# Performance work log

Hardware: AMD Instinct MI355X
Metric: run time of the kernel (lower is better)

Reference implementation:

```python
import jax, jax.numpy as jnp
import numpy as np

B, H, L, D = 2, 16, 2048, 64
SCALE = 1.0 / np.sqrt(D).astype(np.float32)

def setup_inputs() -> dict:
    key = jax.random.key(0)
    kq, kk, kv = jax.random.split(key, 3)
    q = jax.random.normal(kq, (B, H, L, D), dtype=jnp.float32)
    k = jax.random.normal(kk, (B, H, L, D), dtype=jnp.float32)
    v = jax.random.normal(kv, (B, H, L, D), dtype=jnp.float32)
    return {"q": q, "k": k, "v": v}

def reference(q, k, v):
    # scores: [B, H, L_q, L_k]
    attention = jnp.einsum('bhqd,bhkd->bhqk', q, k) * SCALE
    attention = jax.nn.softmax(attention, axis=-1)
    # dropout p=0.0 -> identity
    context = jnp.einsum('bhqk,bhkd->bhqd', attention, v)
    return (context, attention)
```

## Files before the change

kernel.cpp:

```cpp
#include <hip/hip_runtime.h>
#include <stdint.h>


#define L_SEQ 2048
#define D_HEAD 64
#define N_BH   32
#define BQ     64
#define BK     64
#define NT     256

typedef float f32x4 __attribute__((ext_vector_type(4)));
typedef short s16x8 __attribute__((ext_vector_type(8)));

#define MFMA16(A, B, C) __builtin_amdgcn_mfma_f32_16x16x32_bf16((A), (B), (C), 0, 0, 0)

__device__ __forceinline__ unsigned int bf16_rne_u(float x) {
    union { float f; unsigned int u; } c; c.f = x;
    return (c.u + 0x7FFFu + ((c.u >> 16) & 1u)) >> 16;
}
__device__ __forceinline__ float bf16_f32(unsigned int h) {
    union { unsigned int u; float f; } c; c.u = h << 16;
    return c.f;
}

__global__ __launch_bounds__(NT, 2)
void sdpa_mfma_kernel(const float* __restrict__ qg,
                      const float* __restrict__ kg,
                      const float* __restrict__ vg,
                      float* __restrict__ ctx,
                      float* __restrict__ attn)
{
    extern __shared__ char lds[];
    char*  SH = lds;
    char*  SL = lds + 8192;
    float* PS = (float*)(lds + 16384);

    const int t    = threadIdx.x;
    const int lane = t & 63;
    const int wid  = t >> 6;
    const int c    = lane & 15;
    const int g    = lane >> 4;

    const int bh = blockIdx.y;
    const int q0 = blockIdx.x * BQ;

    const float* qb = qg + (size_t)bh * L_SEQ * D_HEAD;
    const float* kb = kg + (size_t)bh * L_SEQ * D_HEAD;
    const float* vb = vg + (size_t)bh * L_SEQ * D_HEAD;

    float* PSw = PS + wid * (16 * 68);

    s16x8 qhi[2], qlo[2];
    {
        const float* qr = qb + (size_t)(q0 + wid * 16 + c) * D_HEAD + g * 8;
        #pragma unroll
        for (int kf = 0; kf < 2; ++kf) {
            float4 a = *(const float4*)(qr + kf * 32);
            float4 b = *(const float4*)(qr + kf * 32 + 4);
            float v[8] = {a.x, a.y, a.z, a.w, b.x, b.y, b.z, b.w};
            #pragma unroll
            for (int i = 0; i < 8; ++i) {
                unsigned int h = bf16_rne_u(v[i]);
                qhi[kf][i] = (short)h;
                qlo[kf][i] = (short)bf16_rne_u(v[i] - bf16_f32(h));
            }
        }
    }

    float rs[4] = {0.f, 0.f, 0.f, 0.f};

    #pragma unroll 1
    for (int kt = 0; kt < L_SEQ / BK; ++kt) {
        __syncthreads();
        {
            const float* kt0 = kb + (size_t)kt * BK * D_HEAD;
            #pragma unroll
            for (int ii = 0; ii < 4; ++ii) {
                int idx = ii * NT + t;
                int r = idx >> 4, c4 = idx & 15;
                float4 val = ((const float4*)(kt0 + (size_t)r * D_HEAD))[c4];
                ushort4 h;
                h.x = (unsigned short)bf16_rne_u(val.x);
                h.y = (unsigned short)bf16_rne_u(val.y);
                h.z = (unsigned short)bf16_rne_u(val.z);
                h.w = (unsigned short)bf16_rne_u(val.w);
                *(ushort4*)(SH + r * 128 + ((c4 * 8) ^ ((r & 7) << 4))) = h;
            }
        }
        __syncthreads();
        #pragma unroll
        for (int cg = 0; cg < 4; ++cg) {
            int j = cg * 16 + c;
            int key = (j & 7) << 4;
            const char* rh = SH + j * 128;
            s16x8 b0 = *(const s16x8*)(rh + ((g * 16) ^ key));
            s16x8 b1 = *(const s16x8*)(rh + ((64 + g * 16) ^ key));
            f32x4 s = {0.f, 0.f, 0.f, 0.f};
            s = MFMA16(qhi[0], b0, s);
            s = MFMA16(qhi[1], b1, s);
            #pragma unroll
            for (int r = 0; r < 4; ++r) rs[r] += __expf(s[r] * 0.125f);
        }
    }

    float inv[4];
    #pragma unroll
    for (int r = 0; r < 4; ++r) {
        float s = rs[r];
        s += __shfl_xor(s, 1); s += __shfl_xor(s, 2);
        s += __shfl_xor(s, 4); s += __shfl_xor(s, 8);
        inv[r] = 1.0f / s;
    }

    float* ab = attn + (size_t)(bh * L_SEQ + q0 + wid * 16) * L_SEQ;
    f32x4 cacc[4];
    #pragma unroll
    for (int cg = 0; cg < 4; ++cg) cacc[cg] = (f32x4){0.f, 0.f, 0.f, 0.f};

    #pragma unroll 1
    for (int kt = 0; kt < L_SEQ / BK; ++kt) {
        __syncthreads();
        {
            const float* kt0 = kb + (size_t)kt * BK * D_HEAD;
            #pragma unroll
            for (int ii = 0; ii < 4; ++ii) {
                int idx = ii * NT + t;
                int r = idx >> 4, c4 = idx & 15;
                float4 val = ((const float4*)(kt0 + (size_t)r * D_HEAD))[c4];
                ushort4 h, l;
                unsigned int hx = bf16_rne_u(val.x), hy = bf16_rne_u(val.y);
                unsigned int hz = bf16_rne_u(val.z), hw = bf16_rne_u(val.w);
                h.x = (unsigned short)hx; h.y = (unsigned short)hy;
                h.z = (unsigned short)hz; h.w = (unsigned short)hw;
                l.x = (unsigned short)bf16_rne_u(val.x - bf16_f32(hx));
                l.y = (unsigned short)bf16_rne_u(val.y - bf16_f32(hy));
                l.z = (unsigned short)bf16_rne_u(val.z - bf16_f32(hz));
                l.w = (unsigned short)bf16_rne_u(val.w - bf16_f32(hw));
                int off = r * 128 + ((c4 * 8) ^ ((r & 7) << 4));
                *(ushort4*)(SH + off) = h;
                *(ushort4*)(SL + off) = l;
            }
        }
        __syncthreads();
        #pragma unroll
        for (int cg = 0; cg < 4; ++cg) {
            int j = cg * 16 + c;
            int key = (j & 7) << 4;
            const char* rh = SH + j * 128;
            const char* rl = SL + j * 128;
            s16x8 bh0 = *(const s16x8*)(rh + ((g * 16) ^ key));
            s16x8 bh1 = *(const s16x8*)(rh + ((64 + g * 16) ^ key));
            s16x8 bl0 = *(const s16x8*)(rl + ((g * 16) ^ key));
            s16x8 bl1 = *(const s16x8*)(rl + ((64 + g * 16) ^ key));
            f32x4 s = {0.f, 0.f, 0.f, 0.f};
            s = MFMA16(qhi[0], bh0, s);
            s = MFMA16(qhi[1], bh1, s);
            s = MFMA16(qlo[0], bh0, s);
            s = MFMA16(qlo[1], bh1, s);
            s = MFMA16(qhi[0], bl0, s);
            s = MFMA16(qhi[1], bl1, s);
            #pragma unroll
            for (int r = 0; r < 4; ++r) {
                float p = __expf(s[r] * 0.125f) * inv[r];
                PSw[(g * 4 + r) * 68 + cg * 16 + c] = p;
            }
        }
        __syncthreads();
        {
            const float* vt0 = vb + (size_t)kt * BK * D_HEAD;
            #pragma unroll
            for (int ii = 0; ii < 2; ++ii) {
                int item = ii * NT + t;
                int d4 = item & 15, j2 = item >> 4;
                const float* r0 = vt0 + (size_t)(2 * j2) * D_HEAD + d4 * 4;
                float4 a = *(const float4*)r0;
                float4 b = *(const float4*)(r0 + D_HEAD);
                float av[4] = {a.x, a.y, a.z, a.w};
                float bv[4] = {b.x, b.y, b.z, b.w};
                #pragma unroll
                for (int i = 0; i < 4; ++i) {
                    int d = d4 * 4 + i;
                    unsigned int h0 = bf16_rne_u(av[i]);
                    unsigned int h1 = bf16_rne_u(bv[i]);
                    unsigned int l0 = bf16_rne_u(av[i] - bf16_f32(h0));
                    unsigned int l1 = bf16_rne_u(bv[i] - bf16_f32(h1));
                    int off = d * 128 + ((4 * j2) ^ ((d & 7) << 4));
                    *(unsigned int*)(SH + off) = h0 | (h1 << 16);
                    *(unsigned int*)(SL + off) = l0 | (l1 << 16);
                }
            }
        }
        __syncthreads();
        #pragma unroll
        for (int it = 0; it < 4; ++it) {
            int r2 = it * 4 + g;
            float4 pv = *(const float4*)(PSw + r2 * 68 + c * 4);
            *(float4*)(ab + (size_t)r2 * L_SEQ + kt * BK + c * 4) = pv;
        }
        s16x8 ph[2], pl[2];
        {
            const float* pr = PSw + c * 68;
            #pragma unroll
            for (int kf = 0; kf < 2; ++kf) {
                float4 a = *(const float4*)(pr + kf * 32 + g * 8);
                float4 b = *(const float4*)(pr + kf * 32 + g * 8 + 4);
                float v[8] = {a.x, a.y, a.z, a.w, b.x, b.y, b.z, b.w};
                #pragma unroll
                for (int i = 0; i < 8; ++i) {
                    unsigned int h = bf16_rne_u(v[i]);
                    ph[kf][i] = (short)h;
                    pl[kf][i] = (short)bf16_rne_u(v[i] - bf16_f32(h));
                }
            }
        }
        #pragma unroll
        for (int cg = 0; cg < 4; ++cg) {
            int d = cg * 16 + c;
            int key = (d & 7) << 4;
            const char* rh = SH + d * 128;
            const char* rl = SL + d * 128;
            s16x8 vh0 = *(const s16x8*)(rh + ((g * 16) ^ key));
            s16x8 vh1 = *(const s16x8*)(rh + ((64 + g * 16) ^ key));
            s16x8 vl0 = *(const s16x8*)(rl + ((g * 16) ^ key));
            s16x8 vl1 = *(const s16x8*)(rl + ((64 + g * 16) ^ key));
            f32x4 cc = cacc[cg];
            cc = MFMA16(ph[0], vh0, cc);
            cc = MFMA16(ph[1], vh1, cc);
            cc = MFMA16(pl[0], vh0, cc);
            cc = MFMA16(pl[1], vh1, cc);
            cc = MFMA16(ph[0], vl0, cc);
            cc = MFMA16(ph[1], vl1, cc);
            cacc[cg] = cc;
        }
    }

    float* cb = ctx + (size_t)(bh * L_SEQ + q0 + wid * 16) * D_HEAD;
    #pragma unroll
    for (int cg = 0; cg < 4; ++cg) {
        #pragma unroll
        for (int r = 0; r < 4; ++r) {
            cb[(size_t)(g * 4 + r) * D_HEAD + cg * 16 + c] = cacc[cg][r];
        }
    }
}

extern "C" void kernel_launch(void* const* d_in, const int* in_sizes, int n_in,
                              void* d_out, int out_size, void* d_ws, size_t ws_size,
                              hipStream_t stream) {
    const float* q = (const float*)d_in[0];
    const float* k = (const float*)d_in[1];
    const float* v = (const float*)d_in[2];
    float* ctx  = (float*)d_out;
    float* attn = ctx + (size_t)N_BH * L_SEQ * D_HEAD;

    dim3 grid(L_SEQ / BQ, N_BH);
    size_t smem = 16384 + (size_t)4 * 16 * 68 * sizeof(float);
    hipLaunchKernelGGL(sdpa_mfma_kernel, grid, dim3(NT), smem, stream,
                       q, k, v, ctx, attn);
}
```

Before: 778.0 us.

## Precompute bf16 hi/lo splits in a prep kernel and prefetch tiles into registers

Adds a prep kernel that converts Q, K and V into bf16 hi/lo planes in workspace once, with V stored transposed. The main kernel then loads these pre-split tiles instead of redoing the conversion in every query block. It also prefetches the next K/V tile into registers while computing the current one, drops two barriers per iteration by giving K and V their own LDS buffers, remaps block indices for L2 locality, and raises the occupancy hint to 3. The cost is an extra launch, extra workspace traffic, and more LDS per block.

```diff
diff --git a/kernel.cpp b/kernel.cpp
--- a/kernel.cpp
+++ b/kernel.cpp
@@ -8,11 +8,13 @@
 #define BQ     64
 #define BK     64
 #define NT     256
+#define NKT    (L_SEQ / BK)
+#define PLANE  ((size_t)N_BH * L_SEQ * D_HEAD)
 
 typedef float f32x4 __attribute__((ext_vector_type(4)));
 typedef short s16x8 __attribute__((ext_vector_type(8)));
 
-#define MFMA16(A, B, C) __builtin_amdgcn_mfma_f32_16x16x32_bf16((A), (B), (C), 0, 0, 0)
+#define MFMA16(A,B,C) __builtin_amdgcn_mfma_f32_16x16x32_bf16((A),(B),(C),0,0,0)
 
 __device__ __forceinline__ unsigned int bf16_rne_u(float x) {
     union { float f; unsigned int u; } c; c.f = x;
@@ -23,76 +25,146 @@
     return c.f;
 }
 
-__global__ __launch_bounds__(NT, 2)
-void sdpa_mfma_kernel(const float* __restrict__ qg,
-                      const float* __restrict__ kg,
-                      const float* __restrict__ vg,
-                      float* __restrict__ ctx,
-                      float* __restrict__ attn)
+__global__ __launch_bounds__(NT)
+void prep_kernel(const float* __restrict__ qg, const float* __restrict__ kg,
+                 const float* __restrict__ vg, unsigned short* __restrict__ W)
+{
+    __shared__ float VT[64][68];
+    const int t = threadIdx.x;
+    const int tile = blockIdx.x, bh = blockIdx.y;
+    const size_t tb = ((size_t)bh * L_SEQ + (size_t)tile * 64) * D_HEAD;
+
+    unsigned short* QH = W;
+    unsigned short* QL = W + PLANE;
+    unsigned short* KH = W + 2 * PLANE;
+    unsigned short* KL = W + 3 * PLANE;
+    unsigned short* VTH = W + 4 * PLANE + (size_t)bh * D_HEAD * L_SEQ;
+    unsigned short* VTL = W + 5 * PLANE + (size_t)bh * D_HEAD * L_SEQ;
+
+    #pragma unroll
+    for (int ii = 0; ii < 4; ++ii) {
+        int idx = ii * NT + t;
+        int r = idx >> 4, c4 = idx & 15;
+        size_t o = tb + (size_t)r * D_HEAD + c4 * 4;
+        {
+            float4 val = *(const float4*)(qg + o);
+            ushort4 h, l;
+            unsigned hx = bf16_rne_u(val.x), hy = bf16_rne_u(val.y);
+            unsigned hz = bf16_rne_u(val.z), hw = bf16_rne_u(val.w);
+            h.x = (unsigned short)hx; h.y = (unsigned short)hy;
+            h.z = (unsigned short)hz; h.w = (unsigned short)hw;
+            l.x = (unsigned short)bf16_rne_u(val.x - bf16_f32(hx));
+            l.y = (unsigned short)bf16_rne_u(val.y - bf16_f32(hy));
+            l.z = (unsigned short)bf16_rne_u(val.z - bf16_f32(hz));
+            l.w = (unsigned short)bf16_rne_u(val.w - bf16_f32(hw));
+            *(ushort4*)(QH + o) = h;
+            *(ushort4*)(QL + o) = l;
+        }
+        {
+            float4 val = *(const float4*)(kg + o);
+            ushort4 h, l;
+            unsigned hx = bf16_rne_u(val.x), hy = bf16_rne_u(val.y);
+            unsigned hz = bf16_rne_u(val.z), hw = bf16_rne_u(val.w);
+            h.x = (unsigned short)hx; h.y = (unsigned short)hy;
+            h.z = (unsigned short)hz; h.w = (unsigned short)hw;
+            l.x = (unsigned short)bf16_rne_u(val.x - bf16_f32(hx));
+            l.y = (unsigned short)bf16_rne_u(val.y - bf16_f32(hy));
+            l.z = (unsigned short)bf16_rne_u(val.z - bf16_f32(hz));
+            l.w = (unsigned short)bf16_rne_u(val.w - bf16_f32(hw));
+            *(ushort4*)(KH + o) = h;
+            *(ushort4*)(KL + o) = l;
+        }
+        {
+            float4 val = *(const float4*)(vg + o);
+            *(float4*)(&VT[r][c4 * 4]) = val;
+        }
+    }
+    __syncthreads();
+    #pragma unroll
+    for (int ii = 0; ii < 2; ++ii) {
+        int item = ii * NT + t;
+        int d = item >> 3, jc = item & 7;
+        s16x8 hv, lv;
+        #pragma unroll
+        for (int j = 0; j < 8; ++j) {
+            float x = VT[jc * 8 + j][d];
+            unsigned h = bf16_rne_u(x);
+            hv[j] = (short)h;
+            lv[j] = (short)bf16_rne_u(x - bf16_f32(h));
+        }
+        size_t o = (size_t)d * L_SEQ + (size_t)tile * 64 + jc * 8;
+        *(s16x8*)(VTH + o) = hv;
+        *(s16x8*)(VTL + o) = lv;
+    }
+}
+
+__global__ __launch_bounds__(NT, 3)
+void sdpa_main(const unsigned short* __restrict__ W,
+               float* __restrict__ ctx, float* __restrict__ attn)
 {
     extern __shared__ char lds[];
-    char*  SH = lds;
-    char*  SL = lds + 8192;
-    float* PS = (float*)(lds + 16384);
-
-    const int t    = threadIdx.x;
-    const int lane = t & 63;
-    const int wid  = t >> 6;
-    const int c    = lane & 15;
-    const int g    = lane >> 4;
-
-    const int bh = blockIdx.y;
-    const int q0 = blockIdx.x * BQ;
-
-    const float* qb = qg + (size_t)bh * L_SEQ * D_HEAD;
-    const float* kb = kg + (size_t)bh * L_SEQ * D_HEAD;
-    const float* vb = vg + (size_t)bh * L_SEQ * D_HEAD;
+    char* KHs = lds;
+    char* KLs = lds + 8192;
+    char* VHs = lds + 16384;
+    char* VLs = lds + 24576;
+    float* PS = (float*)(lds + 32768);
+
+    const int t = threadIdx.x;
+    const int lane = t & 63, wid = t >> 6;
+    const int c = lane & 15, g = lane >> 4;
+
+    const int orig = blockIdx.x;
+    const int wg = (orig & 7) * 128 + (orig >> 3);
+    const int bh = wg >> 5, qb = wg & 31;
+    const int q0 = qb * BQ;
+
+    const unsigned short* QH = W;
+    const unsigned short* QL = W + PLANE;
+    const unsigned short* KHb = W + 2 * PLANE + (size_t)bh * L_SEQ * D_HEAD;
+    const unsigned short* KLb = W + 3 * PLANE + (size_t)bh * L_SEQ * D_HEAD;
+    const unsigned short* VHb = W + 4 * PLANE + (size_t)bh * D_HEAD * L_SEQ;
+    const unsigned short* VLb = W + 5 * PLANE + (size_t)bh * D_HEAD * L_SEQ;
 
     float* PSw = PS + wid * (16 * 68);
 
     s16x8 qhi[2], qlo[2];
     {
-        const float* qr = qb + (size_t)(q0 + wid * 16 + c) * D_HEAD + g * 8;
-        #pragma unroll
-        for (int kf = 0; kf < 2; ++kf) {
-            float4 a = *(const float4*)(qr + kf * 32);
-            float4 b = *(const float4*)(qr + kf * 32 + 4);
-            float v[8] = {a.x, a.y, a.z, a.w, b.x, b.y, b.z, b.w};
-            #pragma unroll
-            for (int i = 0; i < 8; ++i) {
-                unsigned int h = bf16_rne_u(v[i]);
-                qhi[kf][i] = (short)h;
-                qlo[kf][i] = (short)bf16_rne_u(v[i] - bf16_f32(h));
-            }
-        }
-    }
+        size_t qo = ((size_t)bh * L_SEQ + q0 + wid * 16 + c) * D_HEAD + g * 8;
+        qhi[0] = *(const s16x8*)(QH + qo);
+        qhi[1] = *(const s16x8*)(QH + qo + 32);
+        qlo[0] = *(const s16x8*)(QL + qo);
+        qlo[1] = *(const s16x8*)(QL + qo + 32);
+    }
+
+    const int i0 = t, i1 = NT + t;
+    const int r0 = i0 >> 3, c0 = i0 & 7;
+    const int r1 = i1 >> 3, c1 = i1 & 7;
+    const int ld0 = r0 * 128 + ((c0 * 16) ^ ((r0 & 7) << 4));
+    const int ld1 = r1 * 128 + ((c1 * 16) ^ ((r1 & 7) << 4));
+    const size_t ks0 = (size_t)r0 * D_HEAD + c0 * 8;
+    const size_t ks1 = (size_t)r1 * D_HEAD + c1 * 8;
+    const size_t vs0 = (size_t)r0 * L_SEQ + c0 * 8;
+    const size_t vs1 = (size_t)r1 * L_SEQ + c1 * 8;
 
     float rs[4] = {0.f, 0.f, 0.f, 0.f};
+    uint4 pk0 = *(const uint4*)(KHb + ks0);
+    uint4 pk1 = *(const uint4*)(KHb + ks1);
 
     #pragma unroll 1
-    for (int kt = 0; kt < L_SEQ / BK; ++kt) {
+    for (int kt = 0; kt < NKT; ++kt) {
         __syncthreads();
-        {
-            const float* kt0 = kb + (size_t)kt * BK * D_HEAD;
-            #pragma unroll
-            for (int ii = 0; ii < 4; ++ii) {
-                int idx = ii * NT + t;
-                int r = idx >> 4, c4 = idx & 15;
-                float4 val = ((const float4*)(kt0 + (size_t)r * D_HEAD))[c4];
-                ushort4 h;
-                h.x = (unsigned short)bf16_rne_u(val.x);
-                h.y = (unsigned short)bf16_rne_u(val.y);
-                h.z = (unsigned short)bf16_rne_u(val.z);
-                h.w = (unsigned short)bf16_rne_u(val.w);
-                *(ushort4*)(SH + r * 128 + ((c4 * 8) ^ ((r & 7) << 4))) = h;
-            }
-        }
+        *(uint4*)(KHs + ld0) = pk0;
+        *(uint4*)(KHs + ld1) = pk1;
         __syncthreads();
+        if (kt + 1 < NKT) {
+            const unsigned short* kn = KHb + (size_t)(kt + 1) * BK * D_HEAD;
+            pk0 = *(const uint4*)(kn + ks0);
+            pk1 = *(const uint4*)(kn + ks1);
+        }
         #pragma unroll
         for (int cg = 0; cg < 4; ++cg) {
-            int j = cg * 16 + c;
-            int key = (j & 7) << 4;
-            const char* rh = SH + j * 128;
+            int j = cg * 16 + c, key = (j & 7) << 4;
+            const char* rh = KHs + j * 128;
             s16x8 b0 = *(const s16x8*)(rh + ((g * 16) ^ key));
             s16x8 b1 = *(const s16x8*)(rh + ((64 + g * 16) ^ key));
             f32x4 s = {0.f, 0.f, 0.f, 0.f};
@@ -102,7 +174,6 @@
             for (int r = 0; r < 4; ++r) rs[r] += __expf(s[r] * 0.125f);
         }
     }
-
     float inv[4];
     #pragma unroll
     for (int r = 0; r < 4; ++r) {
@@ -112,42 +183,40 @@
         inv[r] = 1.0f / s;
     }
 
-    float* ab = attn + (size_t)(bh * L_SEQ + q0 + wid * 16) * L_SEQ;
+    float* ab = attn + ((size_t)bh * L_SEQ + q0 + wid * 16) * (size_t)L_SEQ;
     f32x4 cacc[4];
     #pragma unroll
     for (int cg = 0; cg < 4; ++cg) cacc[cg] = (f32x4){0.f, 0.f, 0.f, 0.f};
 
+    uint4 kh0 = *(const uint4*)(KHb + ks0), kh1 = *(const uint4*)(KHb + ks1);
+    uint4 kl0 = *(const uint4*)(KLb + ks0), kl1 = *(const uint4*)(KLb + ks1);
+    uint4 vh0 = *(const uint4*)(VHb + vs0), vh1 = *(const uint4*)(VHb + vs1);
+    uint4 vl0 = *(const uint4*)(VLb + vs0), vl1 = *(const uint4*)(VLb + vs1);
+
     #pragma unroll 1
-    for (int kt = 0; kt < L_SEQ / BK; ++kt) {
+    for (int kt = 0; kt < NKT; ++kt) {
         __syncthreads();
-        {
-            const float* kt0 = kb + (size_t)kt * BK * D_HEAD;
-            #pragma unroll
-            for (int ii = 0; ii < 4; ++ii) {
-                int idx = ii * NT + t;
-                int r = idx >> 4, c4 = idx & 15;
-                float4 val = ((const float4*)(kt0 + (size_t)r * D_HEAD))[c4];
-                ushort4 h, l;
-                unsigned int hx = bf16_rne_u(val.x), hy = bf16_rne_u(val.y);
-                unsigned int hz = bf16_rne_u(val.z), hw = bf16_rne_u(val.w);
-                h.x = (unsigned short)hx; h.y = (unsigned short)hy;
-                h.z = (unsigned short)hz; h.w = (unsigned short)hw;
-                l.x = (unsigned short)bf16_rne_u(val.x - bf16_f32(hx));
-                l.y = (unsigned short)bf16_rne_u(val.y - bf16_f32(hy));
-                l.z = (unsigned short)bf16_rne_u(val.z - bf16_f32(hz));
-                l.w = (unsigned short)bf16_rne_u(val.w - bf16_f32(hw));
-                int off = r * 128 + ((c4 * 8) ^ ((r & 7) << 4));
-                *(ushort4*)(SH + off) = h;
-                *(ushort4*)(SL + off) = l;
-            }
-        }
+        *(uint4*)(KHs + ld0) = kh0;  *(uint4*)(KHs + ld1) = kh1;
+        *(uint4*)(KLs + ld0) = kl0;  *(uint4*)(KLs + ld1) = kl1;
+        *(uint4*)(VHs + ld0) = vh0;  *(uint4*)(VHs + ld1) = vh1;
+        *(uint4*)(VLs + ld0) = vl0;  *(uint4*)(VLs + ld1) = vl1;
         __syncthreads();
+        if (kt + 1 < NKT) {
+            const unsigned short* knh = KHb + (size_t)(kt + 1) * BK * D_HEAD;
+            const unsigned short* knl = KLb + (size_t)(kt + 1) * BK * D_HEAD;
+            kh0 = *(const uint4*)(knh + ks0);  kh1 = *(const uint4*)(knh + ks1);
+            kl0 = *(const uint4*)(knl + ks0);  kl1 = *(const uint4*)(knl + ks1);
+            const unsigned short* vnh = VHb + (size_t)(kt + 1) * BK;
+            const unsigned short* vnl = VLb + (size_t)(kt + 1) * BK;
+            vh0 = *(const uint4*)(vnh + vs0);  vh1 = *(const uint4*)(vnh + vs1);
+            vl0 = *(const uint4*)(vnl + vs0);  vl1 = *(const uint4*)(vnl + vs1);
+        }
+
         #pragma unroll
         for (int cg = 0; cg < 4; ++cg) {
-            int j = cg * 16 + c;
-            int key = (j & 7) << 4;
-            const char* rh = SH + j * 128;
-            const char* rl = SL + j * 128;
+            int j = cg * 16 + c, key = (j & 7) << 4;
+            const char* rh = KHs + j * 128;
+            const char* rl = KLs + j * 128;
             s16x8 bh0 = *(const s16x8*)(rh + ((g * 16) ^ key));
             s16x8 bh1 = *(const s16x8*)(rh + ((64 + g * 16) ^ key));
             s16x8 bl0 = *(const s16x8*)(rl + ((g * 16) ^ key));
@@ -165,38 +234,14 @@
                 PSw[(g * 4 + r) * 68 + cg * 16 + c] = p;
             }
         }
-        __syncthreads();
-        {
-            const float* vt0 = vb + (size_t)kt * BK * D_HEAD;
-            #pragma unroll
-            for (int ii = 0; ii < 2; ++ii) {
-                int item = ii * NT + t;
-                int d4 = item & 15, j2 = item >> 4;
-                const float* r0 = vt0 + (size_t)(2 * j2) * D_HEAD + d4 * 4;
-                float4 a = *(const float4*)r0;
-                float4 b = *(const float4*)(r0 + D_HEAD);
-                float av[4] = {a.x, a.y, a.z, a.w};
-                float bv[4] = {b.x, b.y, b.z, b.w};
-                #pragma unroll
-                for (int i = 0; i < 4; ++i) {
-                    int d = d4 * 4 + i;
-                    unsigned int h0 = bf16_rne_u(av[i]);
-                    unsigned int h1 = bf16_rne_u(bv[i]);
-                    unsigned int l0 = bf16_rne_u(av[i] - bf16_f32(h0));
-                    unsigned int l1 = bf16_rne_u(bv[i] - bf16_f32(h1));
-                    int off = d * 128 + ((4 * j2) ^ ((d & 7) << 4));
-                    *(unsigned int*)(SH + off) = h0 | (h1 << 16);
-                    *(unsigned int*)(SL + off) = l0 | (l1 << 16);
-                }
-            }
-        }
-        __syncthreads();
+
         #pragma unroll
         for (int it = 0; it < 4; ++it) {
             int r2 = it * 4 + g;
             float4 pv = *(const float4*)(PSw + r2 * 68 + c * 4);
             *(float4*)(ab + (size_t)r2 * L_SEQ + kt * BK + c * 4) = pv;
         }
+
         s16x8 ph[2], pl[2];
         {
             const float* pr = PSw + c * 68;
@@ -204,37 +249,37 @@
             for (int kf = 0; kf < 2; ++kf) {
                 float4 a = *(const float4*)(pr + kf * 32 + g * 8);
                 float4 b = *(const float4*)(pr + kf * 32 + g * 8 + 4);
-                float v[8] = {a.x, a.y, a.z, a.w, b.x, b.y, b.z, b.w};
+                float vv[8] = {a.x, a.y, a.z, a.w, b.x, b.y, b.z, b.w};
                 #pragma unroll
                 for (int i = 0; i < 8; ++i) {
-                    unsigned int h = bf16_rne_u(v[i]);
+                    unsigned h = bf16_rne_u(vv[i]);
                     ph[kf][i] = (short)h;
-                    pl[kf][i] = (short)bf16_rne_u(v[i] - bf16_f32(h));
+                    pl[kf][i] = (short)bf16_rne_u(vv[i] - bf16_f32(h));
                 }
             }
         }
+
         #pragma unroll
         for (int cg = 0; cg < 4; ++cg) {
-            int d = cg * 16 + c;
-            int key = (d & 7) << 4;
-            const char* rh = SH + d * 128;
-            const char* rl = SL + d * 128;
-            s16x8 vh0 = *(const s16x8*)(rh + ((g * 16) ^ key));
-            s16x8 vh1 = *(const s16x8*)(rh + ((64 + g * 16) ^ key));
-            s16x8 vl0 = *(const s16x8*)(rl + ((g * 16) ^ key));
-            s16x8 vl1 = *(const s16x8*)(rl + ((64 + g * 16) ^ key));
+            int d = cg * 16 + c, key = (d & 7) << 4;
+            const char* rh = VHs + d * 128;
+            const char* rl = VLs + d * 128;
+            s16x8 wh0 = *(const s16x8*)(rh + ((g * 16) ^ key));
+            s16x8 wh1 = *(const s16x8*)(rh + ((64 + g * 16) ^ key));
+            s16x8 wl0 = *(const s16x8*)(rl + ((g * 16) ^ key));
+            s16x8 wl1 = *(const s16x8*)(rl + ((64 + g * 16) ^ key));
             f32x4 cc = cacc[cg];
-            cc = MFMA16(ph[0], vh0, cc);
-            cc = MFMA16(ph[1], vh1, cc);
-            cc = MFMA16(pl[0], vh0, cc);
-            cc = MFMA16(pl[1], vh1, cc);
-            cc = MFMA16(ph[0], vl0, cc);
-            cc = MFMA16(ph[1], vl1, cc);
+            cc = MFMA16(ph[0], wh0, cc);
+            cc = MFMA16(ph[1], wh1, cc);
+            cc = MFMA16(pl[0], wh0, cc);
+            cc = MFMA16(pl[1], wh1, cc);
+            cc = MFMA16(ph[0], wl0, cc);
+            cc = MFMA16(ph[1], wl1, cc);
             cacc[cg] = cc;
         }
     }
 
-    float* cb = ctx + (size_t)(bh * L_SEQ + q0 + wid * 16) * D_HEAD;
+    float* cb = ctx + ((size_t)bh * L_SEQ + q0 + wid * 16) * D_HEAD;
     #pragma unroll
     for (int cg = 0; cg < 4; ++cg) {
         #pragma unroll
@@ -252,9 +297,12 @@
     const float* v = (const float*)d_in[2];
     float* ctx  = (float*)d_out;
     float* attn = ctx + (size_t)N_BH * L_SEQ * D_HEAD;
-
-    dim3 grid(L_SEQ / BQ, N_BH);
-    size_t smem = 16384 + (size_t)4 * 16 * 68 * sizeof(float);
-    hipLaunchKernelGGL(sdpa_mfma_kernel, grid, dim3(NT), smem, stream,
-                       q, k, v, ctx, attn);
-}
+    unsigned short* W = (unsigned short*)d_ws;
+
+    hipLaunchKernelGGL(prep_kernel, dim3(L_SEQ / 64, N_BH), dim3(NT), 0, stream,
+                       q, k, v, W);
+
+    size_t smem = 32768 + (size_t)4 * 16 * 68 * sizeof(float);
+    hipLaunchKernelGGL(sdpa_main, dim3(L_SEQ / BQ * N_BH), dim3(NT), smem, stream,
+                       W, ctx, attn);
+}
```

After: 697.0 us. 1.12x faster.
